# Kernel tuning notes

Hardware: AMD Instinct MI355X
Metric: run time of the kernel (lower is better)

## Reference

```python
import jax, jax.numpy as jnp
import numpy as np

B, N, NOBS, H, A = 8192, 16, 512, 64, 16


def setup_inputs() -> dict:
    key = jax.random.key(0)
    ks = jax.random.split(key, 11)
    s = 0.05
    return {
        "obs": jax.random.normal(ks[0], (B, N, NOBS), dtype=jnp.float32),
        "lstm_h": jnp.zeros((1, 1, H, N), dtype=jnp.float32),
        "lstm_s": jnp.zeros((1, 1, H, N), dtype=jnp.float32),
        "comm": jnp.zeros((1, 1, H, N), dtype=jnp.float32),
        "W1": jax.random.normal(ks[1], (N, 128, NOBS), dtype=jnp.float32) * s,
        "b1": jax.random.normal(ks[2], (N, 128), dtype=jnp.float32) * s,
        "W2": jax.random.normal(ks[3], (N, H, 128), dtype=jnp.float32) * s,
        "b2": jax.random.normal(ks[4], (N, H), dtype=jnp.float32) * s,
        "W_ih": jax.random.normal(ks[5], (4 * H, H), dtype=jnp.float32) * s,
        "W_hh": jax.random.normal(ks[6], (4 * H, H), dtype=jnp.float32) * s,
        "b_ih": jax.random.normal(ks[7], (4 * H,), dtype=jnp.float32) * s,
        "b_hh": jax.random.normal(ks[8], (4 * H,), dtype=jnp.float32) * s,
        "Wd": jax.random.normal(ks[9], (N, A, H), dtype=jnp.float32) * s,
        "bd": jax.random.normal(ks[10], (N, A), dtype=jnp.float32) * s,
    }


def reference(obs, lstm_h, lstm_s, comm, W1, b1, W2, b2, W_ih, W_hh, b_ih, b_hh, Wd, bd):
    # Per-agent encode MLPs, batched over the agent axis. obs: (B,N,NOBS)
    e = jax.nn.relu(jnp.einsum('bni,nhi->bnh', obs, W1) + b1)   # (B,N,128)
    e = jax.nn.relu(jnp.einsum('bnk,nhk->bnh', e, W2) + b2)     # (B,N,H)

    # comm buffer slice comm[:,:,:,i] broadcasts onto (B,1,H); agent axis last.
    comm_t = jnp.transpose(comm[0, 0])                          # (N,H)
    # Original detaches the LSTM input and both states before the shared LSTM.
    x_seq = jax.lax.stop_gradient(e + comm_t[None])             # (B,N,H)
    h0 = jax.lax.stop_gradient(jnp.transpose(lstm_h[0, 0]))     # (N,H)
    c0 = jax.lax.stop_gradient(jnp.transpose(lstm_s[0, 0]))     # (N,H)

    # nn.LSTM given (B,1,H) input treats B as the sequence dim (batch=1):
    # a sequential scan of length B, vectorized here across the N agents.
    bias = b_ih + b_hh
    W_ih_T, W_hh_T = W_ih.T, W_hh.T

    def step(carry, x_t):
        h, c = carry                                            # (N,H) each
        g = x_t @ W_ih_T + h @ W_hh_T + bias                    # (N,4H)
        i_, f_, g_, o_ = jnp.split(g, 4, axis=-1)               # torch order i,f,g,o
        i_ = jax.nn.sigmoid(i_)
        f_ = jax.nn.sigmoid(f_)
        g_ = jnp.tanh(g_)
        o_ = jax.nn.sigmoid(o_)
        c = f_ * c + i_ * g_
        h = o_ * jnp.tanh(c)
        return (h, c), h

    _, hidden = jax.lax.scan(step, (h0, c0), x_seq)             # (B,N,H)

    # Per-agent decode heads -> q values, concatenated over agents.
    q = jnp.einsum('bnh,nah->bna', hidden, Wd) + bd             # (B,N,A)
    return q
```

## Files before the change

### kernel.cpp

```cpp
#include <hip/hip_runtime.h>

#define BSZ   8192
#define NAG   16
#define NOBSZ 512
#define HSZ   64

typedef _Float16 h2 __attribute__((ext_vector_type(2)));

__device__ __forceinline__ float sigmoid_f(float x) { return 1.f / (1.f + __expf(-x)); }
__device__ __forceinline__ float tanh_f(float x)    { float e = __expf(2.f * x); return 1.f - 2.f / (e + 1.f); }

__device__ __forceinline__ void lds_barrier() {
    asm volatile("s_waitcnt lgkmcnt(0)" ::: "memory");
    __builtin_amdgcn_s_barrier();
    asm volatile("" ::: "memory");
}

__global__ __launch_bounds__(256, 2) void encode_kernel(
    const float* __restrict__ obs, const float* __restrict__ comm,
    const float* __restrict__ W1,  const float* __restrict__ b1,
    const float* __restrict__ W2,  const float* __restrict__ b2,
    const float* __restrict__ Wih, const float* __restrict__ bih,
    const float* __restrict__ bhh, float* __restrict__ X)
{
    __shared__ float lds[20480];
    const int n  = blockIdx.y;
    const int bt = blockIdx.x;
    const int t  = threadIdx.x;
    const int ty = t >> 4, tx = t & 15;

    float* sA   = lds;
    float* sW   = lds + 2048;
    float* sW2  = lds;
    float* sE1  = lds + 8192;
    float* sE2  = lds + 16384;
    float* sWih = lds;

    float acc1[4][2][4];
    #pragma unroll
    for (int i = 0; i < 4; i++)
        #pragma unroll
        for (int c = 0; c < 2; c++)
            #pragma unroll
            for (int j = 0; j < 4; j++) acc1[i][c][j] = 0.f;

    const float* obsn = obs + ((size_t)bt * 64 * NAG + n) * NOBSZ;
    const int rA = t >> 2, sgA = t & 3;
    const int hW = t >> 1, sbW = (t & 1) * 4;

    for (int k0 = 0; k0 < NOBSZ; k0 += 32) {
        {
            const float* src = obsn + (size_t)rA * (NAG * NOBSZ) + k0 + sgA * 4;
            float4 v0 = *(const float4*)src;
            float4 v1 = *(const float4*)(src + 16);
            sA[(sgA*4+ 0)*64 + rA] = v0.x; sA[(sgA*4+ 1)*64 + rA] = v0.y;
            sA[(sgA*4+ 2)*64 + rA] = v0.z; sA[(sgA*4+ 3)*64 + rA] = v0.w;
            sA[(sgA*4+16)*64 + rA] = v1.x; sA[(sgA*4+17)*64 + rA] = v1.y;
            sA[(sgA*4+18)*64 + rA] = v1.z; sA[(sgA*4+19)*64 + rA] = v1.w;
        }
        {
            const float* src = W1 + ((size_t)n * 128 + hW) * NOBSZ + k0;
            #pragma unroll
            for (int u = 0; u < 4; u++) {
                float4 v = *(const float4*)(src + (sbW + u) * 4);
                sW[((sbW+u)*4+0)*128 + hW] = v.x;
                sW[((sbW+u)*4+1)*128 + hW] = v.y;
                sW[((sbW+u)*4+2)*128 + hW] = v.z;
                sW[((sbW+u)*4+3)*128 + hW] = v.w;
            }
        }
        __syncthreads();
        #pragma unroll 8
        for (int kk = 0; kk < 32; ++kk) {
            float4 a   = *(const float4*)&sA[kk*64 + ty*4];
            float4 bv0 = *(const float4*)&sW[kk*128 + tx*4];
            float4 bv1 = *(const float4*)&sW[kk*128 + 64 + tx*4];
            float av[4] = {a.x, a.y, a.z, a.w};
            float w0[4] = {bv0.x, bv0.y, bv0.z, bv0.w};
            float w1[4] = {bv1.x, bv1.y, bv1.z, bv1.w};
            #pragma unroll
            for (int i = 0; i < 4; i++) {
                #pragma unroll
                for (int j = 0; j < 4; j++) {
                    acc1[i][0][j] += av[i] * w0[j];
                    acc1[i][1][j] += av[i] * w1[j];
                }
            }
        }
        __syncthreads();
    }
    {
        const float* b1n = b1 + n * 128;
        #pragma unroll
        for (int i = 0; i < 4; i++) {
            int row = ty * 4 + i;
            #pragma unroll
            for (int c = 0; c < 2; c++) {
                #pragma unroll
                for (int j = 0; j < 4; j++) {
                    int col = c * 64 + tx * 4 + j;
                    sE1[col * 64 + row] = fmaxf(acc1[i][c][j] + b1n[col], 0.f);
                }
            }
        }
    }
    {
        const int h = t >> 2, ks = t & 3;
        const float* src = W2 + ((size_t)n * 64 + h) * 128;
        #pragma unroll
        for (int u = 0; u < 8; u++) {
            int s = ks + 4 * u;
            float4 v = *(const float4*)(src + s * 4);
            sW2[(s*4+0)*64 + h] = v.x;
            sW2[(s*4+1)*64 + h] = v.y;
            sW2[(s*4+2)*64 + h] = v.z;
            sW2[(s*4+3)*64 + h] = v.w;
        }
    }
    __syncthreads();

    float acc2[4][4];
    #pragma unroll
    for (int i = 0; i < 4; i++)
        #pragma unroll
        for (int j = 0; j < 4; j++) acc2[i][j] = 0.f;
    #pragma unroll 8
    for (int kk = 0; kk < 128; ++kk) {
        float4 a = *(const float4*)&sE1[kk*64 + ty*4];
        float4 w = *(const float4*)&sW2[kk*64 + tx*4];
        float av[4] = {a.x, a.y, a.z, a.w};
        float wv[4] = {w.x, w.y, w.z, w.w};
        #pragma unroll
        for (int i = 0; i < 4; i++)
            #pragma unroll
            for (int j = 0; j < 4; j++) acc2[i][j] += av[i] * wv[j];
    }
    __syncthreads();
    {
        const float* b2n = b2 + n * 64;
        #pragma unroll
        for (int i = 0; i < 4; i++) {
            int row = ty * 4 + i;
            #pragma unroll
            for (int j = 0; j < 4; j++) {
                int col = tx * 4 + j;
                float v = fmaxf(acc2[i][j] + b2n[col], 0.f) + comm[col * NAG + n];
                sE2[col * 64 + row] = v;
            }
        }
    }
    {
        const float* src = Wih + t * 64;
        #pragma unroll
        for (int u = 0; u < 16; u++) {
            float4 v = *(const float4*)(src + u * 4);
            sWih[(u*4+0)*256 + t] = v.x;
            sWih[(u*4+1)*256 + t] = v.y;
            sWih[(u*4+2)*256 + t] = v.z;
            sWih[(u*4+3)*256 + t] = v.w;
        }
    }
    __syncthreads();

    for (int half = 0; half < 2; ++half) {
        float acc3[4][2][4];
        #pragma unroll
        for (int i = 0; i < 4; i++)
            #pragma unroll
            for (int c = 0; c < 2; c++)
                #pragma unroll
                for (int j = 0; j < 4; j++) acc3[i][c][j] = 0.f;
        #pragma unroll 4
        for (int kk = 0; kk < 64; ++kk) {
            float4 a = *(const float4*)&sE2[kk*64 + ty*4];
            float av[4] = {a.x, a.y, a.z, a.w};
            #pragma unroll
            for (int c = 0; c < 2; c++) {
                int col0 = (half * 2 + c) * 64 + tx * 4;
                float4 w = *(const float4*)&sWih[kk*256 + col0];
                float wv[4] = {w.x, w.y, w.z, w.w};
                #pragma unroll
                for (int i = 0; i < 4; i++)
                    #pragma unroll
                    for (int j = 0; j < 4; j++) acc3[i][c][j] += av[i] * wv[j];
            }
        }
        #pragma unroll
        for (int i = 0; i < 4; i++) {
            int b = bt * 64 + ty * 4 + i;
            float* dst = X + ((size_t)b * NAG + n) * 256;
            #pragma unroll
            for (int c = 0; c < 2; c++) {
                int col0 = (half * 2 + c) * 64 + tx * 4;
                float4 bi = *(const float4*)(bih + col0);
                float4 bh = *(const float4*)(bhh + col0);
                float4 o;
                o.x = acc3[i][c][0] + bi.x + bh.x;
                o.y = acc3[i][c][1] + bi.y + bh.y;
                o.z = acc3[i][c][2] + bi.z + bh.z;
                o.w = acc3[i][c][3] + bi.w + bh.w;
                *(float4*)(dst + col0) = o;
            }
        }
    }
}

__global__ __launch_bounds__(256, 1) void scan_kernel(
    const float* __restrict__ X, const float* __restrict__ Whh,
    const float* __restrict__ lstm_h, const float* __restrict__ lstm_s,
    float* __restrict__ hid)
{
    __shared__ __align__(16) _Float16 hbuf[4][64];
    __shared__ float g_lds[2][4][64];
    const int n = blockIdx.x;
    const int t = threadIdx.x;
    const int w = t >> 6;
    const int j = t & 63;

    h2 wreg[32];
    {
        const float* wr = Whh + (size_t)t * 64;
        #pragma unroll
        for (int u = 0; u < 16; u++) {
            float4 v = *(const float4*)(wr + u * 4);
            h2 p0, p1;
            p0.x = (_Float16)v.x; p0.y = (_Float16)v.y;
            p1.x = (_Float16)v.z; p1.y = (_Float16)v.w;
            wreg[2*u+0] = p0;
            wreg[2*u+1] = p1;
        }
    }

    float c = lstm_s[j * NAG + n];
    hbuf[w][j] = (_Float16)lstm_h[j * NAG + n];
    lds_barrier();

    const float* Xp = X + n * 256 + t;
    float*       hp = hid + n * 64 + j;

    float xa[8], xb[8];
    #pragma unroll
    for (int i = 0; i < 8; i++) { xa[i] = Xp[(size_t)i * 4096]; xb[i] = 0.f; }

    const float4* hb4 = (const float4*)hbuf[w];

    for (int b0 = 0; b0 < BSZ; b0 += 8) {
        if (b0 + 8 < BSZ) {
            #pragma unroll
            for (int i = 0; i < 8; i++) xb[i] = Xp[(size_t)(b0 + 8 + i) * 4096];
        }
        #pragma unroll
        for (int i = 0; i < 8; i++) {
            const int p = i & 1;
            float a0 = 0.f, a1 = 0.f, a2 = 0.f, a3 = 0.f;
            #pragma unroll
            for (int u = 0; u < 8; u++) {
                float4 v = hb4[u];
                a0 = __builtin_amdgcn_fdot2(wreg[4*u+0], __builtin_bit_cast(h2, v.x), a0, false);
                a1 = __builtin_amdgcn_fdot2(wreg[4*u+1], __builtin_bit_cast(h2, v.y), a1, false);
                a2 = __builtin_amdgcn_fdot2(wreg[4*u+2], __builtin_bit_cast(h2, v.z), a2, false);
                a3 = __builtin_amdgcn_fdot2(wreg[4*u+3], __builtin_bit_cast(h2, v.w), a3, false);
            }
            float gp  = xa[i] + ((a0 + a1) + (a2 + a3));
            float arg = (w == 2) ? 2.f * gp : gp;
            float sg  = 1.f / (1.f + __expf(-arg));
            float act = (w == 2) ? 2.f * sg - 1.f : sg;
            g_lds[p][w][j] = act;
            lds_barrier();
            float is = g_lds[p][0][j];
            float fs = g_lds[p][1][j];
            float gs = g_lds[p][2][j];
            float os = g_lds[p][3][j];
            c = fs * c + is * gs;
            float hh = os * tanh_f(c);
            hbuf[w][j] = (_Float16)hh;
            if (t < 64) hp[(size_t)(b0 + i) * (NAG * 64)] = hh;
        }
        #pragma unroll
        for (int i = 0; i < 8; i++) xa[i] = xb[i];
    }
}

__global__ __launch_bounds__(256) void decode_kernel(
    const float* __restrict__ hid, const float* __restrict__ Wd,
    const float* __restrict__ bd, float* __restrict__ q)
{
    int g   = blockIdx.x * 256 + threadIdx.x;
    int row = g >> 4;
    int a   = g & 15;
    int n   = row & 15;
    const float4* hr = (const float4*)(hid + (size_t)row * 64);
    const float4* wr = (const float4*)(Wd + ((size_t)n * 16 + a) * 64);
    float s0 = 0.f, s1 = 0.f, s2 = 0.f, s3 = 0.f;
    #pragma unroll
    for (int u = 0; u < 16; u += 4) {
        float4 h0 = hr[u+0], h1 = hr[u+1], h2v = hr[u+2], h3 = hr[u+3];
        float4 w0 = wr[u+0], w1 = wr[u+1], w2 = wr[u+2], w3 = wr[u+3];
        s0 += h0.x*w0.x + h0.y*w0.y + h0.z*w0.z + h0.w*w0.w;
        s1 += h1.x*w1.x + h1.y*w1.y + h1.z*w1.z + h1.w*w1.w;
        s2 += h2v.x*w2.x + h2v.y*w2.y + h2v.z*w2.z + h2v.w*w2.w;
        s3 += h3.x*w3.x + h3.y*w3.y + h3.z*w3.z + h3.w*w3.w;
    }
    q[g] = bd[n * 16 + a] + ((s0 + s1) + (s2 + s3));
}

extern "C" void kernel_launch(void* const* d_in, const int* in_sizes, int n_in,
                              void* d_out, int out_size, void* d_ws, size_t ws_size,
                              hipStream_t stream) {
    const float* obs    = (const float*)d_in[0];
    const float* lstm_h = (const float*)d_in[1];
    const float* lstm_s = (const float*)d_in[2];
    const float* comm   = (const float*)d_in[3];
    const float* W1     = (const float*)d_in[4];
    const float* b1     = (const float*)d_in[5];
    const float* W2     = (const float*)d_in[6];
    const float* b2     = (const float*)d_in[7];
    const float* W_ih   = (const float*)d_in[8];
    const float* W_hh   = (const float*)d_in[9];
    const float* b_ih   = (const float*)d_in[10];
    const float* b_hh   = (const float*)d_in[11];
    const float* Wd     = (const float*)d_in[12];
    const float* bd     = (const float*)d_in[13];
    float* q   = (float*)d_out;

    float* X   = (float*)d_ws;
    float* hid = (float*)d_ws + (size_t)BSZ * NAG * 256;
    (void)in_sizes; (void)n_in; (void)out_size; (void)ws_size;

    encode_kernel<<<dim3(128, 16), 256, 0, stream>>>(obs, comm, W1, b1, W2, b2,
                                                     W_ih, b_ih, b_hh, X);
    scan_kernel<<<16, 256, 0, stream>>>(X, W_hh, lstm_h, lstm_s, hid);
    decode_kernel<<<(BSZ * NAG * 16) / 256, 256, 0, stream>>>(hid, Wd, bd, q);
}
```

Baseline: 3.810 ms.

## Run LSTM scan for all agents in one block using MFMA f16 matmuls

Rewrites the sequential LSTM scan so that a single workgroup handles all 16 agents at once. Each step computes the recurrent gate product with 16x16x32 f16 MFMA instructions, with the X input preloaded into the accumulator. The hidden state is exchanged through LDS as packed halves, which takes two barriers per step. This replaces 16 independent blocks that each did per-thread dot2 reductions, cutting instruction count per step. In exchange the scan now runs on only one CU, so per-step latency (MFMA, transcendentals, two barriers) sets the total time, where before 16 blocks ran in parallel.

```diff
diff --git a/kernel.cpp b/kernel.cpp
--- a/kernel.cpp
+++ b/kernel.cpp
@@ -5,7 +5,9 @@
 #define NOBSZ 512
 #define HSZ   64
 
-typedef _Float16 h2 __attribute__((ext_vector_type(2)));
+typedef _Float16 h2    __attribute__((ext_vector_type(2)));
+typedef _Float16 f16x8 __attribute__((ext_vector_type(8)));
+typedef float    f32x4 __attribute__((ext_vector_type(4)));
 
 __device__ __forceinline__ float sigmoid_f(float x) { return 1.f / (1.f + __expf(-x)); }
 __device__ __forceinline__ float tanh_f(float x)    { float e = __expf(2.f * x); return 1.f - 2.f / (e + 1.f); }
@@ -14,6 +16,11 @@
     asm volatile("s_waitcnt lgkmcnt(0)" ::: "memory");
     __builtin_amdgcn_s_barrier();
     asm volatile("" ::: "memory");
+}
+
+__device__ __forceinline__ int packh2(float x, float y) {
+    h2 p; p.x = (_Float16)x; p.y = (_Float16)y;
+    return __builtin_bit_cast(int, p);
 }
 
 __global__ __launch_bounds__(256, 2) void encode_kernel(
@@ -210,74 +217,111 @@
     const float* __restrict__ lstm_h, const float* __restrict__ lstm_s,
     float* __restrict__ hid)
 {
-    __shared__ __align__(16) _Float16 hbuf[4][64];
-    __shared__ float g_lds[2][4][64];
-    const int n = blockIdx.x;
-    const int t = threadIdx.x;
-    const int w = t >> 6;
-    const int j = t & 63;
-
-    h2 wreg[32];
-    {
-        const float* wr = Whh + (size_t)t * 64;
-        #pragma unroll
-        for (int u = 0; u < 16; u++) {
-            float4 v = *(const float4*)(wr + u * 4);
-            h2 p0, p1;
-            p0.x = (_Float16)v.x; p0.y = (_Float16)v.y;
-            p1.x = (_Float16)v.z; p1.y = (_Float16)v.w;
-            wreg[2*u+0] = p0;
-            wreg[2*u+1] = p1;
-        }
-    }
-
-    float c = lstm_s[j * NAG + n];
-    hbuf[w][j] = (_Float16)lstm_h[j * NAG + n];
-    lds_barrier();
-
-    const float* Xp = X + n * 256 + t;
-    float*       hp = hid + n * 64 + j;
-
-    float xa[8], xb[8];
-    #pragma unroll
-    for (int i = 0; i < 8; i++) { xa[i] = Xp[(size_t)i * 4096]; xb[i] = 0.f; }
-
-    const float4* hb4 = (const float4*)hbuf[w];
-
-    for (int b0 = 0; b0 < BSZ; b0 += 8) {
-        if (b0 + 8 < BSZ) {
-            #pragma unroll
-            for (int i = 0; i < 8; i++) xb[i] = Xp[(size_t)(b0 + 8 + i) * 4096];
-        }
-        #pragma unroll
-        for (int i = 0; i < 8; i++) {
-            const int p = i & 1;
-            float a0 = 0.f, a1 = 0.f, a2 = 0.f, a3 = 0.f;
-            #pragma unroll
-            for (int u = 0; u < 8; u++) {
-                float4 v = hb4[u];
-                a0 = __builtin_amdgcn_fdot2(wreg[4*u+0], __builtin_bit_cast(h2, v.x), a0, false);
-                a1 = __builtin_amdgcn_fdot2(wreg[4*u+1], __builtin_bit_cast(h2, v.y), a1, false);
-                a2 = __builtin_amdgcn_fdot2(wreg[4*u+2], __builtin_bit_cast(h2, v.z), a2, false);
-                a3 = __builtin_amdgcn_fdot2(wreg[4*u+3], __builtin_bit_cast(h2, v.w), a3, false);
-            }
-            float gp  = xa[i] + ((a0 + a1) + (a2 + a3));
-            float arg = (w == 2) ? 2.f * gp : gp;
-            float sg  = 1.f / (1.f + __expf(-arg));
-            float act = (w == 2) ? 2.f * sg - 1.f : sg;
-            g_lds[p][w][j] = act;
-            lds_barrier();
-            float is = g_lds[p][0][j];
-            float fs = g_lds[p][1][j];
-            float gs = g_lds[p][2][j];
-            float os = g_lds[p][3][j];
-            c = fs * c + is * gs;
-            float hh = os * tanh_f(c);
-            hbuf[w][j] = (_Float16)hh;
-            if (t < 64) hp[(size_t)(b0 + i) * (NAG * 64)] = hh;
-        }
-        #pragma unroll
-        for (int i = 0; i < 8; i++) xa[i] = xb[i];
+    __shared__ float g_lds[16][64][4];
+    __shared__ int   hp_lds[16][36];
+    const int t  = threadIdx.x;
+    const int wv = t >> 6;
+    const int l  = t & 63;
+    const int a  = l & 15;
+    const int rg = l >> 4;
+
+    f16x8 afrag[4][2];
+    #pragma unroll
+    for (int mt = 0; mt < 4; mt++)
+        #pragma unroll
+        for (int kt = 0; kt < 2; kt++) {
+            const float* src = Whh + (size_t)(64*wv + mt*16 + a) * 64 + kt*32 + rg*8;
+            float4 v0 = *(const float4*)src;
+            float4 v1 = *(const float4*)(src + 4);
+            f16x8 f;
+            f[0]=(_Float16)v0.x; f[1]=(_Float16)v0.y; f[2]=(_Float16)v0.z; f[3]=(_Float16)v0.w;
+            f[4]=(_Float16)v1.x; f[5]=(_Float16)v1.y; f[6]=(_Float16)v1.z; f[7]=(_Float16)v1.w;
+            afrag[mt][kt] = f;
+        }
+
+    f16x8 bfrag[2];
+    #pragma unroll
+    for (int kt = 0; kt < 2; kt++) {
+        f16x8 f;
+        #pragma unroll
+        for (int e = 0; e < 8; e++) {
+            int k = kt*32 + rg*8 + e;
+            f[e] = (_Float16)lstm_h[k * NAG + a];
+        }
+        bfrag[kt] = f;
+    }
+
+    float cst[4];
+    #pragma unroll
+    for (int r = 0; r < 4; r++) cst[r] = lstm_s[(wv*16 + rg*4 + r) * NAG + a];
+
+    const float* Xb = X + a*256 + 64*wv + rg*4;
+    float*       hq = hid + a*64 + wv*16 + rg*4;
+
+    float4 xa[4], xb[4];
+    #pragma unroll
+    for (int mt = 0; mt < 4; mt++) xa[mt] = *(const float4*)(Xb + mt*16);
+
+    auto step = [&](int b, float4 (&xc)[4]) {
+        f32x4 g[4];
+        #pragma unroll
+        for (int mt = 0; mt < 4; mt++) {
+            g[mt] = __builtin_amdgcn_mfma_f32_16x16x32_f16(
+                        afrag[mt][0], bfrag[0],
+                        __builtin_bit_cast(f32x4, xc[mt]), 0, 0, 0);
+            g[mt] = __builtin_amdgcn_mfma_f32_16x16x32_f16(
+                        afrag[mt][1], bfrag[1], g[mt], 0, 0, 0);
+        }
+        if (wv == 2) {
+            #pragma unroll
+            for (int mt = 0; mt < 4; mt++)
+                #pragma unroll
+                for (int r = 0; r < 4; r++) g[mt][r] = tanh_f(g[mt][r]);
+        } else {
+            #pragma unroll
+            for (int mt = 0; mt < 4; mt++)
+                #pragma unroll
+                for (int r = 0; r < 4; r++) g[mt][r] = sigmoid_f(g[mt][r]);
+        }
+        #pragma unroll
+        for (int mt = 0; mt < 4; mt++)
+            *(float4*)&g_lds[wv*4 + mt][l][0] = __builtin_bit_cast(float4, g[mt]);
+        lds_barrier();
+        f32x4 is = __builtin_bit_cast(f32x4, *(const float4*)&g_lds[0*4 + wv][l][0]);
+        f32x4 fs = __builtin_bit_cast(f32x4, *(const float4*)&g_lds[1*4 + wv][l][0]);
+        f32x4 gs = __builtin_bit_cast(f32x4, *(const float4*)&g_lds[2*4 + wv][l][0]);
+        f32x4 os = __builtin_bit_cast(f32x4, *(const float4*)&g_lds[3*4 + wv][l][0]);
+        float hh[4];
+        #pragma unroll
+        for (int r = 0; r < 4; r++) {
+            cst[r] = fs[r] * cst[r] + is[r] * gs[r];
+            hh[r]  = os[r] * tanh_f(cst[r]);
+        }
+        *(float4*)(hq + (size_t)b * (NAG * HSZ)) =
+            make_float4(hh[0], hh[1], hh[2], hh[3]);
+        int2 pw;
+        pw.x = packh2(hh[0], hh[1]);
+        pw.y = packh2(hh[2], hh[3]);
+        *(int2*)&hp_lds[a][wv*8 + rg*2] = pw;
+        lds_barrier();
+        #pragma unroll
+        for (int kt = 0; kt < 2; kt++) {
+            int4 pk = *(const int4*)&hp_lds[a][kt*16 + rg*4];
+            bfrag[kt] = __builtin_bit_cast(f16x8, pk);
+        }
+    };
+
+    for (int b = 0; b < BSZ; b += 2) {
+        #pragma unroll
+        for (int mt = 0; mt < 4; mt++)
+            xb[mt] = *(const float4*)(Xb + (size_t)(b + 1) * 4096 + mt*16);
+        step(b, xa);
+        if (b + 2 < BSZ) {
+            #pragma unroll
+            for (int mt = 0; mt < 4; mt++)
+                xa[mt] = *(const float4*)(Xb + (size_t)(b + 2) * 4096 + mt*16);
+        }
+        step(b + 1, xb);
     }
 }
 
@@ -329,6 +373,6 @@
 
     encode_kernel<<<dim3(128, 16), 256, 0, stream>>>(obs, comm, W1, b1, W2, b2,
                                                      W_ih, b_ih, b_hh, X);
-    scan_kernel<<<16, 256, 0, stream>>>(X, W_hh, lstm_h, lstm_s, hid);
+    scan_kernel<<<1, 256, 0, stream>>>(X, W_hh, lstm_h, lstm_s, hid);
     decode_kernel<<<(BSZ * NAG * 16) / 256, 256, 0, stream>>>(hid, Wd, bd, q);
 }
```

New measurement: 11.73 ms. 3.08x slower.
